# Kernel optimization log

Measured on AMD Instinct MI355X. Metric: run time of the kernel, lower is better.

The kernel has to match this reference:

```python
import jax, jax.numpy as jnp
import numpy as np
from jax import lax

VOCAB = 32000
D = 64
B = 32
S = 512
DECAY_P = 0.1  # p in rho_t = (1-p)*rho_{t-1} + outer(x_t, x_t)


def setup_inputs() -> dict:
    key = jax.random.key(0)
    k1, k2 = jax.random.split(key)
    x = jax.random.randint(k1, (B, S), 0, VOCAB, dtype=jnp.int64)
    emb = jax.random.normal(k2, (VOCAB, D), dtype=jnp.float32)
    return {"x": x, "emb": emb}


def reference(x, emb):
    # Embedding lookup: [B, S, D]
    content = emb[x]
    # Per-token outer products (projectedRho): [B, S, D, D]
    proj = jnp.einsum('bsi,bsj->bsij', content, content)
    # Initial rho = identity, repeated over batch: [B, D, D]
    init_rho = jnp.broadcast_to(jnp.eye(D, dtype=emb.dtype), (B, D, D))
    decay = jnp.asarray(1.0 - DECAY_P, dtype=emb.dtype)

    def step(rho, p_t):
        rho = rho * decay + p_t  # [B, D, D]
        return rho, rho

    # scan over time axis; proj transposed to [S, B, D, D]
    _, states = lax.scan(step, init_rho, jnp.swapaxes(proj, 0, 1))
    # states: [S, B, D, D] -> return as [B, S, D, D] (stacked list of states)
    return jnp.swapaxes(states, 0, 1)
```

## Files before the change

kernel.cpp:

```cpp
#include <hip/hip_runtime.h>

#define VOCAB 32000
#define D     64
#define B     32
#define S     512
#define NCHUNK 8
#define CLEN   64

typedef float vf4 __attribute__((ext_vector_type(4)));

__global__ __launch_bounds__(256, 4) void qmn_fused(
    const int*  __restrict__ x,
    const float* __restrict__ emb,
    vf4*        __restrict__ out4)
{
    const float DECAY = 0.9f;

    int blk   = blockIdx.x;
    int c     = blk & (NCHUNK - 1);
    int iBase = ((blk >> 3) & 3) * 16;
    int b     = blk >> 5;

    int jq = threadIdx.x & 15;
    int i  = iBase + (threadIdx.x >> 4);

    const int* xb = x + b * S;
    const vf4* embv = (const vf4*)emb;

    vf4 rho;
    int j0 = jq * 4;
    rho.x = (i == j0 + 0) ? 1.0f : 0.0f;
    rho.y = (i == j0 + 1) ? 1.0f : 0.0f;
    rho.z = (i == j0 + 2) ? 1.0f : 0.0f;
    rho.w = (i == j0 + 3) ? 1.0f : 0.0f;

    const int tStart = c * CLEN;

    #pragma unroll 8
    for (int t = 0; t < tStart; ++t) {
        int tok = xb[t];
        float ci = emb[tok * D + i];
        vf4  cj  = embv[tok * (D / 4) + jq];
        rho.x = rho.x * DECAY + ci * cj.x;
        rho.y = rho.y * DECAY + ci * cj.y;
        rho.z = rho.z * DECAY + ci * cj.z;
        rho.w = rho.w * DECAY + ci * cj.w;
    }

    vf4* outp = out4 + (((size_t)(b * S + tStart)) * D + i) * (D / 4) + jq;

    #pragma unroll 4
    for (int tt = 0; tt < CLEN; ++tt) {
        int tok = xb[tStart + tt];
        float ci = emb[tok * D + i];
        vf4  cj  = embv[tok * (D / 4) + jq];
        rho.x = rho.x * DECAY + ci * cj.x;
        rho.y = rho.y * DECAY + ci * cj.y;
        rho.z = rho.z * DECAY + ci * cj.z;
        rho.w = rho.w * DECAY + ci * cj.w;
        __builtin_nontemporal_store(rho, outp);
        outp += D * (D / 4);
    }
}

extern "C" void kernel_launch(void* const* d_in, const int* in_sizes, int n_in,
                              void* d_out, int out_size, void* d_ws, size_t ws_size,
                              hipStream_t stream) {
    const int*   x   = (const int*)d_in[0];
    const float* emb = (const float*)d_in[1];
    vf4* out = (vf4*)d_out;

    qmn_fused<<<B * NCHUNK * 4, 256, 0, stream>>>(x, emb, out);
}
```

Before: 365.4 us.

## Pre-gather embeddings into contiguous workspace before chunked outer-product scan

Adds a separate gather kernel that copies each token's embedding row into a contiguous [B,S,D] workspace buffer. The main scan kernel then reads consecutive rows, so it no longer does a dependent token-index load followed by a random embedding-row gather. The block-index mapping is reordered so the chunk index is the slowest-varying coordinate, and the nontemporal output stores become plain stores. In exchange there is an extra kernel launch and a workspace round trip, and plain stores may pollute the cache on a large write-bound output.

```diff
diff --git a/kernel.cpp b/kernel.cpp
--- a/kernel.cpp
+++ b/kernel.cpp
@@ -9,23 +9,29 @@
 
 typedef float vf4 __attribute__((ext_vector_type(4)));
 
-__global__ __launch_bounds__(256, 4) void qmn_fused(
-    const int*  __restrict__ x,
-    const float* __restrict__ emb,
+__global__ void qmn_gather(const int* __restrict__ x,
+                           const vf4* __restrict__ emb4,
+                           vf4* __restrict__ content4) {
+    int tid = blockIdx.x * blockDim.x + threadIdx.x;
+    int bs  = tid >> 4;
+    int d4  = tid & 15;
+    int tok = x[bs];
+    content4[tid] = emb4[tok * (D / 4) + d4];
+}
+
+__global__ __launch_bounds__(256, 4) void qmn_chunks(
+    const float* __restrict__ content,
     vf4*        __restrict__ out4)
 {
     const float DECAY = 0.9f;
 
     int blk   = blockIdx.x;
-    int c     = blk & (NCHUNK - 1);
-    int iBase = ((blk >> 3) & 3) * 16;
-    int b     = blk >> 5;
+    int c     = blk >> 7;
+    int b     = (blk >> 2) & 31;
+    int iBase = (blk & 3) * 16;
 
     int jq = threadIdx.x & 15;
     int i  = iBase + (threadIdx.x >> 4);
-
-    const int* xb = x + b * S;
-    const vf4* embv = (const vf4*)emb;
 
     vf4 rho;
     int j0 = jq * 4;
@@ -34,13 +40,14 @@
     rho.z = (i == j0 + 2) ? 1.0f : 0.0f;
     rho.w = (i == j0 + 3) ? 1.0f : 0.0f;
 
+    const float* cb  = content + (size_t)b * S * D;
+    const vf4*   cb4 = (const vf4*)cb;
     const int tStart = c * CLEN;
 
     #pragma unroll 8
     for (int t = 0; t < tStart; ++t) {
-        int tok = xb[t];
-        float ci = emb[tok * D + i];
-        vf4  cj  = embv[tok * (D / 4) + jq];
+        float ci = cb[t * D + i];
+        vf4   cj = cb4[t * (D / 4) + jq];
         rho.x = rho.x * DECAY + ci * cj.x;
         rho.y = rho.y * DECAY + ci * cj.y;
         rho.z = rho.z * DECAY + ci * cj.z;
@@ -51,14 +58,14 @@
 
     #pragma unroll 4
     for (int tt = 0; tt < CLEN; ++tt) {
-        int tok = xb[tStart + tt];
-        float ci = emb[tok * D + i];
-        vf4  cj  = embv[tok * (D / 4) + jq];
+        int t = tStart + tt;
+        float ci = cb[t * D + i];
+        vf4   cj = cb4[t * (D / 4) + jq];
         rho.x = rho.x * DECAY + ci * cj.x;
         rho.y = rho.y * DECAY + ci * cj.y;
         rho.z = rho.z * DECAY + ci * cj.z;
         rho.w = rho.w * DECAY + ci * cj.w;
-        __builtin_nontemporal_store(rho, outp);
+        *outp = rho;
         outp += D * (D / 4);
     }
 }
@@ -70,5 +77,10 @@
     const float* emb = (const float*)d_in[1];
     vf4* out = (vf4*)d_out;
 
-    qmn_fused<<<B * NCHUNK * 4, 256, 0, stream>>>(x, emb, out);
+    float* content = (float*)d_ws;
+
+    qmn_gather<<<B * S * (D / 4) / 256, 256, 0, stream>>>(
+        x, (const vf4*)emb, (vf4*)content);
+
+    qmn_chunks<<<B * NCHUNK * 4, 256, 0, stream>>>(content, out);
 }
```

After: 294.0 us. 1.24x faster.
